# Performance work log

Measured on AMD Instinct MI355X. Metric: run time of the kernel, lower is better.

## Reference

```python
import jax, jax.numpy as jnp
import numpy as np


def setup_inputs() -> dict:
    key = jax.random.key(0)
    kq, kk, kv = jax.random.split(key, 3)
    B, H, S, D = 2, 8, 4096, 64
    return {
        "query": jax.random.normal(kq, (B, H, S, D), dtype=jnp.float32),
        "key": jax.random.normal(kk, (B, H, S, D), dtype=jnp.float32),
        "value": jax.random.normal(kv, (B, H, S, D), dtype=jnp.float32),
    }


def reference(query, key, value):
    # NOTE: the torch source overwrites sqrt(d) with d, so the divisor is D, not sqrt(D).
    d = query.shape[-1]
    # score: [B, H, S_q, S_k]
    score = jnp.einsum("bhqd,bhkd->bhqk", query, key) / d
    relu = jax.nn.relu(score)  # no softmax / row normalization
    out = jnp.einsum("bhqk,bhkd->bhqd", relu, value)
    return out
```

## Files before the change

kernel.cpp:

```cpp
#include <hip/hip_runtime.h>
#include <hip/hip_bf16.h>
#include <stdint.h>


#define NH 16
#define SEQ 4096
#define DD 64
#define HE (SEQ*DD)
#define HB (HE*2)
#define Q16_OFF 0
#define K16_OFF (NH*HB)
#define V16_OFF (2*NH*HB)
#define WS_NEED (3*NH*HB)

typedef __attribute__((ext_vector_type(8)))  short    bf16x8;
typedef __attribute__((ext_vector_type(16))) float    f32x16;
typedef __attribute__((ext_vector_type(4)))  uint32_t u32x4;

__device__ inline uint32_t f2bf1(float f) {
  return (uint32_t)__builtin_bit_cast(unsigned short, __float2bfloat16(f));
}
__device__ inline uint32_t pack2bf(float a, float b) {
  return f2bf1(a) | (f2bf1(b) << 16);
}
__device__ inline uint32_t cvtpk(float lo, float hi) {
  uint32_t r;
  asm("v_cvt_pk_bf16_f32 %0, %1, %2" : "=v"(r) : "v"(lo), "v"(hi));
  return r;
}
__device__ inline uint32_t relu2(uint32_t w) {
  uint32_t r;
  asm("v_pk_max_f16 %0, %1, 0" : "=v"(r) : "v"(w));
  return r;
}

__global__ __launch_bounds__(256) void prepass_kernel(const float* __restrict__ Q,
                                                      const float* __restrict__ K,
                                                      const float* __restrict__ V,
                                                      char* __restrict__ ws) {
  __shared__ float vt[64*65];
  int bx = blockIdx.x, tid = threadIdx.x;
  if (bx < 2048) {
    int head = bx >> 7, qg = bx & 127;
    int r31 = tid & 31, c = tid >> 5;
    const float4* s = (const float4*)(Q + (size_t)head*HE + ((size_t)(qg*32 + r31))*64 + c*8);
    float4 a = s[0], b = s[1];
    const float sc = 1.0f/64.0f;
    u32x4 o;
    o.x = pack2bf(a.x*sc, a.y*sc);
    o.y = pack2bf(a.z*sc, a.w*sc);
    o.z = pack2bf(b.x*sc, b.y*sc);
    o.w = pack2bf(b.z*sc, b.w*sc);
    char* tb = ws + Q16_OFF + (size_t)head*HB;
    *(u32x4*)(tb + ((qg*4 + (c >> 1))*1024) + ((c & 1)*32 + r31)*16) = o;
  } else if (bx < 3072) {
    int tile = bx - 2048;
    int head = tile >> 6, t = tile & 63;
    int r = tid >> 2, c0 = (tid & 3) * 16;
    const float4* s4 = (const float4*)(K + (size_t)head*HE + ((size_t)(t*64 + r))*64 + c0);
    float4 f0 = s4[0], f1 = s4[1], f2 = s4[2], f3 = s4[3];
    u32x4 c_lo, c_hi;
    c_lo.x = pack2bf(f0.x, f0.y); c_lo.y = pack2bf(f0.z, f0.w);
    c_lo.z = pack2bf(f1.x, f1.y); c_lo.w = pack2bf(f1.z, f1.w);
    c_hi.x = pack2bf(f2.x, f2.y); c_hi.y = pack2bf(f2.z, f2.w);
    c_hi.z = pack2bf(f3.x, f3.y); c_hi.w = pack2bf(f3.z, f3.w);
    char* tb = ws + K16_OFF + ((size_t)head*64 + t)*8192;
    char* chunk = tb + ((r >> 5)*4 + (tid & 3))*1024 + (r & 31)*16;
    *(u32x4*)(chunk)       = c_lo;
    *(u32x4*)(chunk + 512) = c_hi;
  } else {
    int tile = bx - 3072;
    int head = tile >> 6, t = tile & 63;
    int k = tid >> 2, c0 = (tid & 3)*16;
    const float4* s4 = (const float4*)(V + (size_t)head*HE + ((size_t)(t*64 + k))*64 + c0);
    float4 f0 = s4[0], f1 = s4[1], f2 = s4[2], f3 = s4[3];
    float tmp[16] = {f0.x,f0.y,f0.z,f0.w, f1.x,f1.y,f1.z,f1.w,
                     f2.x,f2.y,f2.z,f2.w, f3.x,f3.y,f3.z,f3.w};
    #pragma unroll
    for (int j = 0; j < 16; ++j) vt[k*65 + c0 + j] = tmp[j];
    __syncthreads();
    int d = tid >> 2, k0 = (tid & 3)*16;
    float v2[16];
    #pragma unroll
    for (int j = 0; j < 16; ++j) v2[j] = vt[(k0 + j)*65 + d];
    u32x4 c_lo, c_hi;
    c_lo.x = pack2bf(v2[0],  v2[1]);  c_lo.y = pack2bf(v2[2],  v2[3]);
    c_lo.z = pack2bf(v2[4],  v2[5]);  c_lo.w = pack2bf(v2[6],  v2[7]);
    c_hi.x = pack2bf(v2[8],  v2[9]);  c_hi.y = pack2bf(v2[10], v2[11]);
    c_hi.z = pack2bf(v2[12], v2[13]); c_hi.w = pack2bf(v2[14], v2[15]);
    char* tb = ws + V16_OFF + ((size_t)head*64 + t)*8192;
    char* chunk = tb + ((d >> 5)*4 + (tid & 3))*1024 + (d & 31)*16;
    *(u32x4*)(chunk)       = c_lo;
    *(u32x4*)(chunk + 512) = c_hi;
  }
}

__global__ __launch_bounds__(256, 2) void attn_kernel(const char* __restrict__ ws,
                                                      float* __restrict__ out) {
  __shared__ __align__(16) char lds[2*2*16384];
  int bid = blockIdx.x;
  int bx = (bid & 7) * 64 + (bid >> 3);
  int head = bx >> 5, qblk = bx & 31;
  int tid = threadIdx.x;
  int lane = tid & 63, w = tid >> 6;
  int l31 = lane & 31, h = lane >> 5;
  int g  = w >> 1;
  int wg = w & 1;

  const char* q16   = ws + Q16_OFF + (size_t)head*HB;
  const char* kbase = ws + K16_OFF + (size_t)head*HB + (size_t)g*32*8192;
  const char* vbase = ws + V16_OFF + (size_t)head*HB + (size_t)g*32*8192;

  int qg0 = qblk*4 + wg*2;
  bf16x8 qf[2][4];
  #pragma unroll
  for (int m = 0; m < 2; ++m)
    #pragma unroll
    for (int t = 0; t < 4; ++t)
      qf[m][t] = *(const bf16x8*)(q16 + ((size_t)((qg0 + m)*4 + t))*1024 + lane*16);

  f32x16 kZero;
  #pragma unroll
  for (int i = 0; i < 16; ++i) kZero[i] = 0.f;

  f32x16 o[2][2];
  #pragma unroll
  for (int m = 0; m < 2; ++m)
    #pragma unroll
    for (int nd = 0; nd < 2; ++nd)
      #pragma unroll
      for (int i = 0; i < 16; ++i) o[m][nd][i] = 0.f;

  auto stage = [&](int kt) {
    const char* ktile = kbase + (size_t)kt*8192;
    const char* vtile = vbase + (size_t)kt*8192;
    char* lk = lds + (size_t)(g*2 + (kt & 1))*16384;
    char* lv = lk + 8192;
    #pragma unroll
    for (int c = 0; c < 4; ++c) {
      int off = (wg*4 + c)*1024;
      __builtin_amdgcn_global_load_lds(
          (const __attribute__((address_space(1))) void*)(ktile + off + lane*16),
          (__attribute__((address_space(3))) void*)(lk + off), 16, 0, 0);
      __builtin_amdgcn_global_load_lds(
          (const __attribute__((address_space(1))) void*)(vtile + off + lane*16),
          (__attribute__((address_space(3))) void*)(lv + off), 16, 0, 0);
    }
  };

  stage(0);
  #pragma unroll 1
  for (int kt = 0; kt < 32; ++kt) {
    asm volatile("s_waitcnt vmcnt(0)" ::: "memory");
    __builtin_amdgcn_s_barrier();
    if (kt + 1 < 32) stage(kt + 1);

    const char* lk = lds + (size_t)(g*2 + (kt & 1))*16384;
    const char* lv = lk + 8192;

    bf16x8 kf[2][4];
    #pragma unroll
    for (int i = 0; i < 8; ++i)
      kf[i >> 2][i & 3] = *(const bf16x8*)(lk + i*1024 + lane*16);

    f32x16 st[2][2];
    __builtin_amdgcn_s_setprio(1);
    #pragma unroll
    for (int n = 0; n < 2; ++n)
      #pragma unroll
      for (int m = 0; m < 2; ++m)
        st[m][n] = __builtin_amdgcn_mfma_f32_32x32x16_bf16(kf[n][0], qf[m][0], kZero, 0, 0, 0);
    #pragma unroll
    for (int t = 1; t < 4; ++t)
      #pragma unroll
      for (int n = 0; n < 2; ++n)
        #pragma unroll
        for (int m = 0; m < 2; ++m)
          st[m][n] = __builtin_amdgcn_mfma_f32_32x32x16_bf16(kf[n][t], qf[m][t], st[m][n], 0, 0, 0);
    __builtin_amdgcn_s_setprio(0);

    bf16x8 vf[2][4];
    #pragma unroll
    for (int i = 0; i < 8; ++i)
      vf[i >> 2][i & 3] = *(const bf16x8*)(lv + i*1024 + lane*16);

    bf16x8 pa[2][4];
    auto packg = [&](int n, int kn) {
      #pragma unroll
      for (int m = 0; m < 2; ++m) {
        uint32_t w0 = cvtpk(st[m][n][kn*8+0], st[m][n][kn*8+1]);
        uint32_t w1 = cvtpk(st[m][n][kn*8+2], st[m][n][kn*8+3]);
        uint32_t w2 = cvtpk(st[m][n][kn*8+4], st[m][n][kn*8+5]);
        uint32_t w3 = cvtpk(st[m][n][kn*8+6], st[m][n][kn*8+7]);
        asm("v_permlane32_swap_b32 %0, %1" : "+v"(w0), "+v"(w2));
        asm("v_permlane32_swap_b32 %0, %1" : "+v"(w1), "+v"(w3));
        union { uint32_t u[4]; bf16x8 v; } pk;
        pk.u[0] = relu2(w0);
        pk.u[1] = relu2(w1);
        pk.u[2] = relu2(w2);
        pk.u[3] = relu2(w3);
        pa[m][n*2 + kn] = pk.v;
      }
    };
    auto pvks = [&](int ks) {
      #pragma unroll
      for (int m = 0; m < 2; ++m)
        #pragma unroll
        for (int nd = 0; nd < 2; ++nd)
          o[m][nd] = __builtin_amdgcn_mfma_f32_32x32x16_bf16(pa[m][ks], vf[nd][ks], o[m][nd], 0, 0, 0);
    };

    packg(0, 0);
    packg(0, 1);
    __builtin_amdgcn_s_setprio(1);
    pvks(0);
    __builtin_amdgcn_s_setprio(0);
    packg(1, 0);
    __builtin_amdgcn_s_setprio(1);
    pvks(1);
    __builtin_amdgcn_s_setprio(0);
    packg(1, 1);
    __builtin_amdgcn_s_setprio(1);
    pvks(2);
    pvks(3);
    __builtin_amdgcn_s_setprio(0);
  }

  __syncthreads();
  float* red = (float*)lds;
  if (g == 1) {
    #pragma unroll
    for (int m = 0; m < 2; ++m)
      #pragma unroll
      for (int nd = 0; nd < 2; ++nd)
        #pragma unroll
        for (int r = 0; r < 16; ++r) {
          int ql = wg*64 + m*32 + (r & 3) + 8*(r >> 2) + 4*h;
          red[ql*64 + nd*32 + l31] = o[m][nd][r];
        }
  }
  __syncthreads();
  if (g == 0) {
    float* outh = out + (size_t)head*HE;
    #pragma unroll
    for (int m = 0; m < 2; ++m)
      #pragma unroll
      for (int nd = 0; nd < 2; ++nd)
        #pragma unroll
        for (int r = 0; r < 16; ++r) {
          int ql = wg*64 + m*32 + (r & 3) + 8*(r >> 2) + 4*h;
          float v = o[m][nd][r] + red[ql*64 + nd*32 + l31];
          outh[(size_t)(qblk*128 + ql)*64 + nd*32 + l31] = v;
        }
  }
}

extern "C" void kernel_launch(void* const* d_in, const int* in_sizes, int n_in,
                              void* d_out, int out_size, void* d_ws, size_t ws_size,
                              hipStream_t stream) {
  if (n_in < 3 || ws_size < (size_t)WS_NEED) return;
  const float* Q = (const float*)d_in[0];
  const float* K = (const float*)d_in[1];
  const float* V = (const float*)d_in[2];
  float* out = (float*)d_out;
  char* ws = (char*)d_ws;
  hipLaunchKernelGGL(prepass_kernel, dim3(4096), dim3(256), 0, stream, Q, K, V, ws);
  hipLaunchKernelGGL(attn_kernel,    dim3(512),  dim3(256), 0, stream, ws, out);
}
```

Before: 78.94 us.

## Drop split-K across wave groups; each wave owns more queries, loads V directly

Each block now covers 256 queries with 4 waves, each wave handling 64 queries over the full key range. This removes the two-group key split and its LDS reduction at the end. K tiles go through a 4-deep LDS ring prefetched two tiles ahead with a partial vmcnt wait. V fragments are loaded straight from global into registers one iteration early. The grid halves to 256 blocks, which is fewer than the 256 CUs times 2 needed for full occupancy, so latency hiding may drop. V loads also no longer share LDS reuse.

Measured after the change: 92.06 us. 16.6% more time.

```diff
diff --git a/kernel.cpp b/kernel.cpp
--- a/kernel.cpp
+++ b/kernel.cpp
@@ -97,21 +97,19 @@
 
 __global__ __launch_bounds__(256, 2) void attn_kernel(const char* __restrict__ ws,
                                                       float* __restrict__ out) {
-  __shared__ __align__(16) char lds[2*2*16384];
+  __shared__ __align__(16) char lds[4*8192];
   int bid = blockIdx.x;
-  int bx = (bid & 7) * 64 + (bid >> 3);
-  int head = bx >> 5, qblk = bx & 31;
+  int bx = (bid & 7) * 32 + (bid >> 3);
+  int head = bx >> 4, qblk = bx & 15;
   int tid = threadIdx.x;
   int lane = tid & 63, w = tid >> 6;
   int l31 = lane & 31, h = lane >> 5;
-  int g  = w >> 1;
-  int wg = w & 1;
 
   const char* q16   = ws + Q16_OFF + (size_t)head*HB;
-  const char* kbase = ws + K16_OFF + (size_t)head*HB + (size_t)g*32*8192;
-  const char* vbase = ws + V16_OFF + (size_t)head*HB + (size_t)g*32*8192;
-
-  int qg0 = qblk*4 + wg*2;
+  const char* kbase = ws + K16_OFF + (size_t)head*HB;
+  const char* vbase = ws + V16_OFF + (size_t)head*HB;
+
+  int qg0 = qblk*8 + w*2;
   bf16x8 qf[2][4];
   #pragma unroll
   for (int m = 0; m < 2; ++m)
@@ -131,33 +129,36 @@
       #pragma unroll
       for (int i = 0; i < 16; ++i) o[m][nd][i] = 0.f;
 
-  auto stage = [&](int kt) {
+  bf16x8 vf[2][4];
+
+  auto stageK = [&](int kt) {
     const char* ktile = kbase + (size_t)kt*8192;
-    const char* vtile = vbase + (size_t)kt*8192;
-    char* lk = lds + (size_t)(g*2 + (kt & 1))*16384;
-    char* lv = lk + 8192;
-    #pragma unroll
-    for (int c = 0; c < 4; ++c) {
-      int off = (wg*4 + c)*1024;
+    char* lk = lds + (size_t)(kt & 3)*8192;
+    #pragma unroll
+    for (int c = 0; c < 2; ++c) {
+      int off = (w*2 + c)*1024;
       __builtin_amdgcn_global_load_lds(
           (const __attribute__((address_space(1))) void*)(ktile + off + lane*16),
           (__attribute__((address_space(3))) void*)(lk + off), 16, 0, 0);
-      __builtin_amdgcn_global_load_lds(
-          (const __attribute__((address_space(1))) void*)(vtile + off + lane*16),
-          (__attribute__((address_space(3))) void*)(lv + off), 16, 0, 0);
     }
   };
-
-  stage(0);
+  auto loadV = [&](int kt) {
+    const char* vp = vbase + (size_t)kt*8192;
+    #pragma unroll
+    for (int i = 0; i < 8; ++i)
+      vf[i >> 2][i & 3] = *(const bf16x8*)(vp + i*1024 + lane*16);
+  };
+
+  stageK(0);
+  stageK(1);
+  loadV(0);
   #pragma unroll 1
-  for (int kt = 0; kt < 32; ++kt) {
-    asm volatile("s_waitcnt vmcnt(0)" ::: "memory");
+  for (int kt = 0; kt < 64; ++kt) {
+    asm volatile("s_waitcnt vmcnt(10)" ::: "memory");
     __builtin_amdgcn_s_barrier();
-    if (kt + 1 < 32) stage(kt + 1);
-
-    const char* lk = lds + (size_t)(g*2 + (kt & 1))*16384;
-    const char* lv = lk + 8192;
-
+    if (kt + 2 < 64) stageK(kt + 2);
+
+    const char* lk = lds + (size_t)(kt & 3)*8192;
     bf16x8 kf[2][4];
     #pragma unroll
     for (int i = 0; i < 8; ++i)
@@ -178,11 +179,6 @@
         for (int m = 0; m < 2; ++m)
           st[m][n] = __builtin_amdgcn_mfma_f32_32x32x16_bf16(kf[n][t], qf[m][t], st[m][n], 0, 0, 0);
     __builtin_amdgcn_s_setprio(0);
-
-    bf16x8 vf[2][4];
-    #pragma unroll
-    for (int i = 0; i < 8; ++i)
-      vf[i >> 2][i & 3] = *(const bf16x8*)(lv + i*1024 + lane*16);
 
     bf16x8 pa[2][4];
     auto packg = [&](int n, int kn) {
@@ -224,35 +220,20 @@
     pvks(2);
     pvks(3);
     __builtin_amdgcn_s_setprio(0);
+
+    if (kt + 1 < 64) loadV(kt + 1);
   }
 
-  __syncthreads();
-  float* red = (float*)lds;
-  if (g == 1) {
-    #pragma unroll
-    for (int m = 0; m < 2; ++m)
-      #pragma unroll
-      for (int nd = 0; nd < 2; ++nd)
-        #pragma unroll
-        for (int r = 0; r < 16; ++r) {
-          int ql = wg*64 + m*32 + (r & 3) + 8*(r >> 2) + 4*h;
-          red[ql*64 + nd*32 + l31] = o[m][nd][r];
-        }
-  }
-  __syncthreads();
-  if (g == 0) {
-    float* outh = out + (size_t)head*HE;
-    #pragma unroll
-    for (int m = 0; m < 2; ++m)
-      #pragma unroll
-      for (int nd = 0; nd < 2; ++nd)
-        #pragma unroll
-        for (int r = 0; r < 16; ++r) {
-          int ql = wg*64 + m*32 + (r & 3) + 8*(r >> 2) + 4*h;
-          float v = o[m][nd][r] + red[ql*64 + nd*32 + l31];
-          outh[(size_t)(qblk*128 + ql)*64 + nd*32 + l31] = v;
-        }
-  }
+  float* outh = out + (size_t)head*HE;
+  #pragma unroll
+  for (int m = 0; m < 2; ++m)
+    #pragma unroll
+    for (int nd = 0; nd < 2; ++nd)
+      #pragma unroll
+      for (int r = 0; r < 16; ++r) {
+        int ql = w*64 + m*32 + (r & 3) + 8*(r >> 2) + 4*h;
+        outh[(size_t)(qblk*256 + ql)*64 + nd*32 + l31] = o[m][nd][r];
+      }
 }
 
 extern "C" void kernel_launch(void* const* d_in, const int* in_sizes, int n_in,
@@ -265,5 +246,5 @@
   float* out = (float*)d_out;
   char* ws = (char*)d_ws;
   hipLaunchKernelGGL(prepass_kernel, dim3(4096), dim3(256), 0, stream, Q, K, V, ws);
-  hipLaunchKernelGGL(attn_kernel,    dim3(512),  dim3(256), 0, stream, ws, out);
-}
+  hipLaunchKernelGGL(attn_kernel,    dim3(256),  dim3(256), 0, stream, ws, out);
+}
```
